# Kernel optimization log

Measured on AMD Instinct MI355X. Metric: run time of the kernel, lower is better.

The kernel has to match this reference:

```python
import jax, jax.numpy as jnp
import numpy as np

N_NODES = 50000
N_EDGES = 400000
NODE_FEAT = 32
HIDDEN = 256
ACTION_DIM = 6
NUM_GRAPHS = 64


def setup_inputs() -> dict:
    key = jax.random.key(0)
    ks = jax.random.split(key, 9)
    x = jax.random.normal(ks[0], (N_NODES, NODE_FEAT), dtype=jnp.float32)
    edge_index = jax.random.randint(ks[1], (2, N_EDGES), 0, N_NODES, dtype=jnp.int32)
    batch = jnp.sort(jax.random.randint(ks[2], (N_NODES,), 0, NUM_GRAPHS, dtype=jnp.int32))
    # GCNConv weights (PyG stores Linear without bias + separate bias term;
    # here W is [in, out] so h = x @ W)
    s1 = 1.0 / np.sqrt(NODE_FEAT)
    s2 = 1.0 / np.sqrt(HIDDEN)
    W1 = jax.random.uniform(ks[3], (NODE_FEAT, HIDDEN), jnp.float32, -s1, s1)
    b1 = jnp.zeros((HIDDEN,), jnp.float32)
    W2 = jax.random.uniform(ks[4], (HIDDEN, HIDDEN), jnp.float32, -s2, s2)
    b2 = jnp.zeros((HIDDEN,), jnp.float32)
    Wf = jax.random.uniform(ks[5], (HIDDEN, 2 * ACTION_DIM), jnp.float32, -s2, s2)
    bf = jax.random.uniform(ks[6], (2 * ACTION_DIM,), jnp.float32, -s2, s2)
    return {"x": x, "edge_index": edge_index, "batch": batch,
            "W1": W1, "b1": b1, "W2": W2, "b2": b2, "Wf": Wf, "bf": bf}


def gcn_conv(x, src, dst, deg_inv_sqrt, W, b, num_nodes):
    # PyG GCNConv: h = x @ W, messages h[src] * norm scattered to dst, + bias.
    h = x @ W  # [N, out]
    norm = deg_inv_sqrt[src] * deg_inv_sqrt[dst]  # [E+N]
    msgs = h[src] * norm[:, None]  # [E+N, out]  (dominant memory traffic)
    out = jax.ops.segment_sum(msgs, dst, num_segments=num_nodes)
    return out + b


def reference(x, edge_index, batch, W1, b1, W2, b2, Wf, bf):
    num_nodes = x.shape[0]
    loop = jnp.arange(num_nodes, dtype=edge_index.dtype)
    src = jnp.concatenate([edge_index[0], loop])  # self-loops, PyG default
    dst = jnp.concatenate([edge_index[1], loop])
    deg = jax.ops.segment_sum(jnp.ones_like(dst, dtype=x.dtype), dst,
                              num_segments=num_nodes)  # >=1 due to self-loops
    deg_inv_sqrt = jax.lax.rsqrt(deg)

    h = jax.nn.relu(gcn_conv(x, src, dst, deg_inv_sqrt, W1, b1, num_nodes))
    h = jax.nn.relu(gcn_conv(h, src, dst, deg_inv_sqrt, W2, b2, num_nodes))

    # global_mean_pool over graph ids
    sums = jax.ops.segment_sum(h, batch, num_segments=NUM_GRAPHS)
    counts = jax.ops.segment_sum(jnp.ones((num_nodes,), x.dtype), batch,
                                 num_segments=NUM_GRAPHS)
    pooled = sums / jnp.maximum(counts, 1.0)[:, None]  # [G, HIDDEN]

    mls = pooled @ Wf + bf  # [G, 2*ACTION_DIM]
    mean, log_std = jnp.split(mls, 2, axis=-1)
    std = jnp.exp(jnp.clip(log_std, -20.0, 2.0))
    return mean, std
```

## Files before the change

### kernel.cpp

```cpp
#include <hip/hip_runtime.h>
#include <math.h>

#define NN 50000
#define FEAT 32
#define HID 256
#define NGRAPH 64
#define CAP 64

typedef __attribute__((ext_vector_type(8))) short bfrag;
typedef __attribute__((ext_vector_type(4))) float f32x4;

__device__ __forceinline__ float bf2f(unsigned short u) {
    union { unsigned int i; float f; } v; v.i = ((unsigned int)u) << 16; return v.f;
}
__device__ __forceinline__ unsigned short f2bf(float f) {
    union { float f; unsigned int i; } v; v.f = f;
    unsigned int r = v.i + 0x7fffu + ((v.i >> 16) & 1u);
    return (unsigned short)(r >> 16);
}

__global__ void k_zero(float4* __restrict__ p, int n16) {
    int i = blockIdx.x * blockDim.x + threadIdx.x;
    if (i < n16) p[i] = make_float4(0.f, 0.f, 0.f, 0.f);
}

__global__ void k_setup(const int* __restrict__ src, const int* __restrict__ dst,
                        const int* __restrict__ batch,
                        int* __restrict__ counter, int* __restrict__ csr,
                        int* __restrict__ starts, int E, int N) {
    int e = blockIdx.x * blockDim.x + threadIdx.x;
    if (e < E) {
        int d = dst[e];
        int p = atomicAdd(&counter[d], 1);
        if (p < CAP) csr[d * CAP + p] = src[e];
    }
    if (e < N) {
        int b = batch[e];
        int prev = (e == 0) ? -1 : batch[e - 1];
        if (b != prev) {
            for (int g = prev + 1; g <= b; ++g) starts[g] = e;
        }
        if (e == N - 1) {
            for (int g = b + 1; g <= NGRAPH; ++g) starts[g] = N;
        }
    }
}

__global__ void k_disps(const float* __restrict__ x, const int* __restrict__ cnt,
                        float* __restrict__ dis, unsigned short* __restrict__ xp, int N) {
    int id = blockIdx.x * blockDim.x + threadIdx.x;
    if (id >= N * FEAT) return;
    int node = id >> 5;
    float dn = rsqrtf((float)(cnt[node] + 1));
    if ((id & 31) == 0) dis[node] = dn;
    xp[id] = f2bf(x[id] * dn);
}

__device__ __forceinline__ void pack_w(const float* __restrict__ W,
                                       unsigned short* __restrict__ Wp, int K, int o) {
    int j    = o & 7;
    int lane = (o >> 3) & 63;
    int rest = o >> 9;
    int nst  = K >> 5;
    int ks   = rest & (nst - 1);
    int nb   = rest / nst;
    int n = nb * 16 + (lane & 15);
    int k = ks * 32 + (lane >> 4) * 8 + j;
    Wp[o] = f2bf(W[(size_t)k * HID + n]);
}
__global__ void k_cvtw(const float* __restrict__ W1, const float* __restrict__ W2,
                       unsigned short* __restrict__ W1p, unsigned short* __restrict__ W2p) {
    int o = blockIdx.x * blockDim.x + threadIdx.x;
    if (o < FEAT * HID) pack_w(W1, W1p, FEAT, o);
    int o2 = o - FEAT * HID;
    if (o2 >= 0 && o2 < HID * HID) pack_w(W2, W2p, HID, o2);
}

__global__ void k_aggx(const unsigned short* __restrict__ xp, const int* __restrict__ cnt,
                       const int* __restrict__ csr, const float* __restrict__ dis,
                       unsigned short* __restrict__ out, int N) {
    int node = blockIdx.x * 8 + (threadIdx.x >> 5);
    if (node >= N) return;
    int col = threadIdx.x & 31;
    float acc = bf2f(xp[(size_t)node * FEAT + col]);
    int e = cnt[node]; if (e > CAP) e = CAP;
    const int* lst = &csr[(size_t)node * CAP];
    int i = 0;
    for (; i + 4 <= e; i += 4) {
        int4 s4 = *(const int4*)&lst[i];
        float v0 = bf2f(xp[(size_t)s4.x * FEAT + col]);
        float v1 = bf2f(xp[(size_t)s4.y * FEAT + col]);
        float v2 = bf2f(xp[(size_t)s4.z * FEAT + col]);
        float v3 = bf2f(xp[(size_t)s4.w * FEAT + col]);
        acc += (v0 + v1) + (v2 + v3);
    }
    for (; i < e; ++i) acc += bf2f(xp[(size_t)lst[i] * FEAT + col]);
    out[(size_t)node * FEAT + col] = f2bf(acc * dis[node]);
}

__global__ void k_aggh(const unsigned short* __restrict__ h, const int* __restrict__ cnt,
                       const int* __restrict__ csr, const float* __restrict__ dis,
                       unsigned short* __restrict__ out, int N) {
    int wid = (int)((blockIdx.x * (size_t)blockDim.x + threadIdx.x) >> 6);
    if (wid >= N) return;
    int lane = threadIdx.x & 63;
    int c0 = lane * 4;

    ushort4 hv = *(const ushort4*)&h[(size_t)wid * HID + c0];
    float a0 = bf2f(hv.x), a1 = bf2f(hv.y), a2 = bf2f(hv.z), a3 = bf2f(hv.w);

    int e = cnt[wid]; if (e > CAP) e = CAP;
    const int* lst = &csr[(size_t)wid * CAP];
    int i = 0;
    for (; i + 8 <= e; i += 8) {
        int4 sa = *(const int4*)&lst[i];
        int4 sb = *(const int4*)&lst[i + 4];
        ushort4 v0 = *(const ushort4*)&h[(size_t)sa.x * HID + c0];
        ushort4 v1 = *(const ushort4*)&h[(size_t)sa.y * HID + c0];
        ushort4 v2 = *(const ushort4*)&h[(size_t)sa.z * HID + c0];
        ushort4 v3 = *(const ushort4*)&h[(size_t)sa.w * HID + c0];
        ushort4 v4 = *(const ushort4*)&h[(size_t)sb.x * HID + c0];
        ushort4 v5 = *(const ushort4*)&h[(size_t)sb.y * HID + c0];
        ushort4 v6 = *(const ushort4*)&h[(size_t)sb.z * HID + c0];
        ushort4 v7 = *(const ushort4*)&h[(size_t)sb.w * HID + c0];
        a0 += ((bf2f(v0.x) + bf2f(v1.x)) + (bf2f(v2.x) + bf2f(v3.x)))
            + ((bf2f(v4.x) + bf2f(v5.x)) + (bf2f(v6.x) + bf2f(v7.x)));
        a1 += ((bf2f(v0.y) + bf2f(v1.y)) + (bf2f(v2.y) + bf2f(v3.y)))
            + ((bf2f(v4.y) + bf2f(v5.y)) + (bf2f(v6.y) + bf2f(v7.y)));
        a2 += ((bf2f(v0.z) + bf2f(v1.z)) + (bf2f(v2.z) + bf2f(v3.z)))
            + ((bf2f(v4.z) + bf2f(v5.z)) + (bf2f(v6.z) + bf2f(v7.z)));
        a3 += ((bf2f(v0.w) + bf2f(v1.w)) + (bf2f(v2.w) + bf2f(v3.w)))
            + ((bf2f(v4.w) + bf2f(v5.w)) + (bf2f(v6.w) + bf2f(v7.w)));
    }
    for (; i + 4 <= e; i += 4) {
        int4 s4 = *(const int4*)&lst[i];
        ushort4 v0 = *(const ushort4*)&h[(size_t)s4.x * HID + c0];
        ushort4 v1 = *(const ushort4*)&h[(size_t)s4.y * HID + c0];
        ushort4 v2 = *(const ushort4*)&h[(size_t)s4.z * HID + c0];
        ushort4 v3 = *(const ushort4*)&h[(size_t)s4.w * HID + c0];
        a0 += (bf2f(v0.x) + bf2f(v1.x)) + (bf2f(v2.x) + bf2f(v3.x));
        a1 += (bf2f(v0.y) + bf2f(v1.y)) + (bf2f(v2.y) + bf2f(v3.y));
        a2 += (bf2f(v0.z) + bf2f(v1.z)) + (bf2f(v2.z) + bf2f(v3.z));
        a3 += (bf2f(v0.w) + bf2f(v1.w)) + (bf2f(v2.w) + bf2f(v3.w));
    }
    for (; i < e; ++i) {
        ushort4 v = *(const ushort4*)&h[(size_t)lst[i] * HID + c0];
        a0 += bf2f(v.x); a1 += bf2f(v.y); a2 += bf2f(v.z); a3 += bf2f(v.w);
    }
    float dn = dis[wid];
    ushort4 o;
    o.x = f2bf(a0 * dn); o.y = f2bf(a1 * dn); o.z = f2bf(a2 * dn); o.w = f2bf(a3 * dn);
    *(ushort4*)&out[(size_t)wid * HID + c0] = o;
}

__global__ __launch_bounds__(256, 4)
void k_mmf(const unsigned short* __restrict__ A, const unsigned short* __restrict__ Wp,
           const float* __restrict__ bias, const float* __restrict__ scale,
           unsigned short* __restrict__ C, int M, int K, int lgK) {
    __shared__ unsigned short lds[64 * 264];
    int tid  = threadIdx.x;
    int lane = tid & 63;
    int wid  = tid >> 6;
    int l15  = lane & 15;
    int lq   = lane >> 4;
    int row0 = blockIdx.x * 64;

    const int P = K + 8;
    int iters = (64 * K) >> 11;
    for (int it = 0; it < iters; ++it) {
        int flat = (it * 256 + tid) * 8;
        int row = flat >> lgK;
        int col = flat & (K - 1);
        bfrag v = {0, 0, 0, 0, 0, 0, 0, 0};
        int gr = row0 + row;
        if (gr < M) v = *(const bfrag*)&A[(size_t)gr * K + col];
        *(bfrag*)&lds[row * P + col] = v;
    }
    __syncthreads();

    int nsteps = K >> 5;
    f32x4 acc[4][4];
#pragma unroll
    for (int mi = 0; mi < 4; ++mi)
#pragma unroll
        for (int ni = 0; ni < 4; ++ni) acc[mi][ni] = (f32x4){0.f, 0.f, 0.f, 0.f};

    for (int ks = 0; ks < nsteps; ++ks) {
        bfrag fb[4];
#pragma unroll
        for (int ni = 0; ni < 4; ++ni) {
            size_t off = (((size_t)(wid * 4 + ni) * nsteps + ks) * 64 + lane) * 8;
            fb[ni] = *(const bfrag*)&Wp[off];
        }
        bfrag fa[4];
        int koff = ks * 32 + lq * 8;
#pragma unroll
        for (int mi = 0; mi < 4; ++mi)
            fa[mi] = *(const bfrag*)&lds[(mi * 16 + l15) * P + koff];
#pragma unroll
        for (int mi = 0; mi < 4; ++mi)
#pragma unroll
            for (int ni = 0; ni < 4; ++ni)
                acc[mi][ni] = __builtin_amdgcn_mfma_f32_16x16x32_bf16(fb[ni], fa[mi], acc[mi][ni], 0, 0, 0);
    }

    float4 bv[4];
#pragma unroll
    for (int ni = 0; ni < 4; ++ni)
        bv[ni] = *(const float4*)&bias[(wid * 4 + ni) * 16 + lq * 4];
    float sv[4];
#pragma unroll
    for (int mi = 0; mi < 4; ++mi) {
        int gr = row0 + mi * 16 + l15;
        sv[mi] = (gr < M) ? scale[gr] : 0.f;
    }

    __syncthreads();
#pragma unroll
    for (int mi = 0; mi < 4; ++mi) {
#pragma unroll
        for (int ni = 0; ni < 4; ++ni) {
            const float* bp = (const float*)&bv[ni];
            ushort4 o;
            o.x = f2bf(fmaxf(acc[mi][ni][0] + bp[0], 0.f) * sv[mi]);
            o.y = f2bf(fmaxf(acc[mi][ni][1] + bp[1], 0.f) * sv[mi]);
            o.z = f2bf(fmaxf(acc[mi][ni][2] + bp[2], 0.f) * sv[mi]);
            o.w = f2bf(fmaxf(acc[mi][ni][3] + bp[3], 0.f) * sv[mi]);
            *(ushort4*)&lds[(mi * 16 + l15) * 264 + (wid * 4 + ni) * 16 + lq * 4] = o;
        }
    }
    __syncthreads();

#pragma unroll
    for (int i = 0; i < 8; ++i) {
        int F = (i * 256 + tid) * 8;
        int row = F >> 8;
        int col = F & 255;
        int gr = row0 + row;
        if (gr < M) {
            bfrag v = *(const bfrag*)&lds[row * 264 + col];
            *(bfrag*)&C[(size_t)gr * HID + col] = v;
        }
    }
}

__global__ __launch_bounds__(256, 4)
void k_mmfp(const unsigned short* __restrict__ A, const unsigned short* __restrict__ Wp,
            const float* __restrict__ bias, const int* __restrict__ batch,
            float* __restrict__ pooled, int M) {
    __shared__ unsigned short lds[64 * 264];
    __shared__ int bshare[64];
    const int K = HID;
    int tid  = threadIdx.x;
    int lane = tid & 63;
    int wid  = tid >> 6;
    int l15  = lane & 15;
    int lq   = lane >> 4;
    int row0 = blockIdx.x * 64;

    if (tid < 64) {
        int gr = row0 + tid;
        bshare[tid] = (gr < M) ? batch[gr] : -1;
    }

    const int P = K + 8;
    for (int it = 0; it < 8; ++it) {
        int flat = (it * 256 + tid) * 8;
        int row = flat >> 8;
        int col = flat & 255;
        bfrag v = {0, 0, 0, 0, 0, 0, 0, 0};
        int gr = row0 + row;
        if (gr < M) v = *(const bfrag*)&A[(size_t)gr * K + col];
        *(bfrag*)&lds[row * P + col] = v;
    }
    __syncthreads();

    f32x4 acc[4][4];
#pragma unroll
    for (int mi = 0; mi < 4; ++mi)
#pragma unroll
        for (int ni = 0; ni < 4; ++ni) acc[mi][ni] = (f32x4){0.f, 0.f, 0.f, 0.f};

    for (int ks = 0; ks < 8; ++ks) {
        bfrag fb[4];
#pragma unroll
        for (int ni = 0; ni < 4; ++ni) {
            size_t off = (((size_t)(wid * 4 + ni) * 8 + ks) * 64 + lane) * 8;
            fb[ni] = *(const bfrag*)&Wp[off];
        }
        bfrag fa[4];
        int koff = ks * 32 + lq * 8;
#pragma unroll
        for (int mi = 0; mi < 4; ++mi)
            fa[mi] = *(const bfrag*)&lds[(mi * 16 + l15) * P + koff];
#pragma unroll
        for (int mi = 0; mi < 4; ++mi)
#pragma unroll
            for (int ni = 0; ni < 4; ++ni)
                acc[mi][ni] = __builtin_amdgcn_mfma_f32_16x16x32_bf16(fb[ni], fa[mi], acc[mi][ni], 0, 0, 0);
    }

    float4 bv[4];
#pragma unroll
    for (int ni = 0; ni < 4; ++ni)
        bv[ni] = *(const float4*)&bias[(wid * 4 + ni) * 16 + lq * 4];

    __syncthreads();
#pragma unroll
    for (int mi = 0; mi < 4; ++mi) {
#pragma unroll
        for (int ni = 0; ni < 4; ++ni) {
            const float* bp = (const float*)&bv[ni];
            ushort4 o;
            o.x = f2bf(fmaxf(acc[mi][ni][0] + bp[0], 0.f));
            o.y = f2bf(fmaxf(acc[mi][ni][1] + bp[1], 0.f));
            o.z = f2bf(fmaxf(acc[mi][ni][2] + bp[2], 0.f));
            o.w = f2bf(fmaxf(acc[mi][ni][3] + bp[3], 0.f));
            *(ushort4*)&lds[(mi * 16 + l15) * 264 + (wid * 4 + ni) * 16 + lq * 4] = o;
        }
    }
    __syncthreads();

    int c = tid;
    float pacc = 0.f;
    int cur = bshare[0];
    for (int r = 0; r < 64; ++r) {
        int g = bshare[r];
        if (g != cur) {
            if (cur >= 0) atomicAdd(&pooled[(size_t)cur * HID + c], pacc);
            pacc = 0.f; cur = g;
        }
        pacc += bf2f(lds[r * 264 + c]);
    }
    if (cur >= 0) atomicAdd(&pooled[(size_t)cur * HID + c], pacc);
}

__global__ void k_head(const float* __restrict__ pooled, const int* __restrict__ starts,
                       const float* __restrict__ Wf, const float* __restrict__ bf,
                       float* __restrict__ out) {
    int t = blockIdx.x * blockDim.x + threadIdx.x;
    if (t >= NGRAPH * 12) return;
    int g = t / 12, j = t % 12;
    float cntf = (float)(starts[g + 1] - starts[g]);
    float inv = 1.f / fmaxf(cntf, 1.f);
    float s = 0.f;
    for (int k = 0; k < HID; ++k) s += pooled[(size_t)g * HID + k] * Wf[k * 12 + j];
    s = s * inv + bf[j];
    if (j < 6) {
        out[g * 6 + j] = s;
    } else {
        float ls = fminf(fmaxf(s, -20.f), 2.f);
        out[NGRAPH * 6 + g * 6 + (j - 6)] = expf(ls);
    }
}

extern "C" void kernel_launch(void* const* d_in, const int* in_sizes, int n_in,
                              void* d_out, int out_size, void* d_ws, size_t ws_size,
                              hipStream_t stream) {
    const float* x     = (const float*)d_in[0];
    const int*   ei    = (const int*)d_in[1];
    const int*   batch = (const int*)d_in[2];
    const float* W1    = (const float*)d_in[3];
    const float* b1    = (const float*)d_in[4];
    const float* W2    = (const float*)d_in[5];
    const float* b2    = (const float*)d_in[6];
    const float* Wf    = (const float*)d_in[7];
    const float* bfv   = (const float*)d_in[8];
    float* out = (float*)d_out;

    const int E = in_sizes[1] / 2;
    const int N = in_sizes[2];
    const int* srcp = ei;
    const int* dstp = ei + E;

    char* ws = (char*)d_ws;
    const size_t OFF_CTR    = 0;
    const size_t OFF_POOLED = 200192;
    const size_t ZERO_BYTES = 265728;
    const size_t OFF_STARTS = 265728;
    const size_t OFF_DIS    = 266240;
    const size_t OFF_W1P    = 466432;
    const size_t OFF_W2P    = 482816;
    const size_t OFF_CSR    = 613888;
    const size_t OFF_XP     = 13413888;
    const size_t OFF_AGGX   = 16613888;
    const size_t OFF_H1     = 19813888;
    const size_t OFF_G      = 45413888;

    int*            ctr    = (int*)(ws + OFF_CTR);
    float*          pooled = (float*)(ws + OFF_POOLED);
    int*            starts = (int*)(ws + OFF_STARTS);
    float*          dis    = (float*)(ws + OFF_DIS);
    unsigned short* W1p    = (unsigned short*)(ws + OFF_W1P);
    unsigned short* W2p    = (unsigned short*)(ws + OFF_W2P);
    int*            csr    = (int*)(ws + OFF_CSR);
    unsigned short* xp     = (unsigned short*)(ws + OFF_XP);
    unsigned short* aggX   = (unsigned short*)(ws + OFF_AGGX);
    unsigned short* h1     = (unsigned short*)(ws + OFF_H1);
    unsigned short* g      = (unsigned short*)(ws + OFF_G);

    const int T = 256;
    k_zero<<<(265728 / 16 + T - 1) / T, T, 0, stream>>>((float4*)ws, 265728 / 16);
    k_setup<<<(E + T - 1) / T, T, 0, stream>>>(srcp, dstp, batch, ctr, csr, starts, E, N);
    k_disps<<<(N * FEAT + T - 1) / T, T, 0, stream>>>(x, ctr, dis, xp, N);
    k_cvtw<<<((FEAT + HID) * HID + T - 1) / T, T, 0, stream>>>(W1, W2, W1p, W2p);

    k_aggx<<<(N + 7) / 8, T, 0, stream>>>(xp, ctr, csr, dis, aggX, N);
    k_mmf<<<(N + 63) / 64, T, 0, stream>>>(aggX, W1p, b1, dis, h1, N, FEAT, 5);

    k_aggh<<<(N * 64 + T - 1) / T, T, 0, stream>>>(h1, ctr, csr, dis, g, N);
    k_mmfp<<<(N + 63) / 64, T, 0, stream>>>(g, W2p, b2, batch, pooled, N);

    k_head<<<3, T, 0, stream>>>(pooled, starts, Wf, bfv, out);
}
```

Baseline: 128.4 us.

## Fuse neighbor aggregation into GEMM kernels and merge zero with weight packing

Moves the gather-sum aggregation for both GCN layers directly into the MFMA GEMM kernels, writing the aggregated rows straight into LDS instead of round-tripping them through global buffers. It also folds the workspace zeroing into the weight-packing kernel, which cuts the launch count. Memory traffic for the intermediate aggX and g buffers and two launches go away. The trade-off is that the fused kernels run with only 782 blocks, and the gather latency now sits ahead of the MFMA work inside each block, so latency hiding and parallelism for the memory-bound gather may get worse.

Result: slower. 138.8 us (+8.1%).

```diff
diff --git a/kernel.cpp b/kernel.cpp
--- a/kernel.cpp
+++ b/kernel.cpp
@@ -17,43 +17,6 @@
     union { float f; unsigned int i; } v; v.f = f;
     unsigned int r = v.i + 0x7fffu + ((v.i >> 16) & 1u);
     return (unsigned short)(r >> 16);
-}
-
-__global__ void k_zero(float4* __restrict__ p, int n16) {
-    int i = blockIdx.x * blockDim.x + threadIdx.x;
-    if (i < n16) p[i] = make_float4(0.f, 0.f, 0.f, 0.f);
-}
-
-__global__ void k_setup(const int* __restrict__ src, const int* __restrict__ dst,
-                        const int* __restrict__ batch,
-                        int* __restrict__ counter, int* __restrict__ csr,
-                        int* __restrict__ starts, int E, int N) {
-    int e = blockIdx.x * blockDim.x + threadIdx.x;
-    if (e < E) {
-        int d = dst[e];
-        int p = atomicAdd(&counter[d], 1);
-        if (p < CAP) csr[d * CAP + p] = src[e];
-    }
-    if (e < N) {
-        int b = batch[e];
-        int prev = (e == 0) ? -1 : batch[e - 1];
-        if (b != prev) {
-            for (int g = prev + 1; g <= b; ++g) starts[g] = e;
-        }
-        if (e == N - 1) {
-            for (int g = b + 1; g <= NGRAPH; ++g) starts[g] = N;
-        }
-    }
-}
-
-__global__ void k_disps(const float* __restrict__ x, const int* __restrict__ cnt,
-                        float* __restrict__ dis, unsigned short* __restrict__ xp, int N) {
-    int id = blockIdx.x * blockDim.x + threadIdx.x;
-    if (id >= N * FEAT) return;
-    int node = id >> 5;
-    float dn = rsqrtf((float)(cnt[node] + 1));
-    if ((id & 31) == 0) dis[node] = dn;
-    xp[id] = f2bf(x[id] * dn);
 }
 
 __device__ __forceinline__ void pack_w(const float* __restrict__ W,
@@ -68,95 +31,54 @@
     int k = ks * 32 + (lane >> 4) * 8 + j;
     Wp[o] = f2bf(W[(size_t)k * HID + n]);
 }
-__global__ void k_cvtw(const float* __restrict__ W1, const float* __restrict__ W2,
+
+__global__ void k_prep(float4* __restrict__ zp, int n16,
+                       const float* __restrict__ W1, const float* __restrict__ W2,
                        unsigned short* __restrict__ W1p, unsigned short* __restrict__ W2p) {
-    int o = blockIdx.x * blockDim.x + threadIdx.x;
-    if (o < FEAT * HID) pack_w(W1, W1p, FEAT, o);
-    int o2 = o - FEAT * HID;
+    int i = blockIdx.x * blockDim.x + threadIdx.x;
+    if (i < n16) zp[i] = make_float4(0.f, 0.f, 0.f, 0.f);
+    if (i < FEAT * HID) pack_w(W1, W1p, FEAT, i);
+    int o2 = i - FEAT * HID;
     if (o2 >= 0 && o2 < HID * HID) pack_w(W2, W2p, HID, o2);
 }
 
-__global__ void k_aggx(const unsigned short* __restrict__ xp, const int* __restrict__ cnt,
-                       const int* __restrict__ csr, const float* __restrict__ dis,
-                       unsigned short* __restrict__ out, int N) {
-    int node = blockIdx.x * 8 + (threadIdx.x >> 5);
-    if (node >= N) return;
-    int col = threadIdx.x & 31;
-    float acc = bf2f(xp[(size_t)node * FEAT + col]);
-    int e = cnt[node]; if (e > CAP) e = CAP;
-    const int* lst = &csr[(size_t)node * CAP];
-    int i = 0;
-    for (; i + 4 <= e; i += 4) {
-        int4 s4 = *(const int4*)&lst[i];
-        float v0 = bf2f(xp[(size_t)s4.x * FEAT + col]);
-        float v1 = bf2f(xp[(size_t)s4.y * FEAT + col]);
-        float v2 = bf2f(xp[(size_t)s4.z * FEAT + col]);
-        float v3 = bf2f(xp[(size_t)s4.w * FEAT + col]);
-        acc += (v0 + v1) + (v2 + v3);
-    }
-    for (; i < e; ++i) acc += bf2f(xp[(size_t)lst[i] * FEAT + col]);
-    out[(size_t)node * FEAT + col] = f2bf(acc * dis[node]);
-}
-
-__global__ void k_aggh(const unsigned short* __restrict__ h, const int* __restrict__ cnt,
-                       const int* __restrict__ csr, const float* __restrict__ dis,
-                       unsigned short* __restrict__ out, int N) {
-    int wid = (int)((blockIdx.x * (size_t)blockDim.x + threadIdx.x) >> 6);
-    if (wid >= N) return;
-    int lane = threadIdx.x & 63;
-    int c0 = lane * 4;
-
-    ushort4 hv = *(const ushort4*)&h[(size_t)wid * HID + c0];
-    float a0 = bf2f(hv.x), a1 = bf2f(hv.y), a2 = bf2f(hv.z), a3 = bf2f(hv.w);
-
-    int e = cnt[wid]; if (e > CAP) e = CAP;
-    const int* lst = &csr[(size_t)wid * CAP];
-    int i = 0;
-    for (; i + 8 <= e; i += 8) {
-        int4 sa = *(const int4*)&lst[i];
-        int4 sb = *(const int4*)&lst[i + 4];
-        ushort4 v0 = *(const ushort4*)&h[(size_t)sa.x * HID + c0];
-        ushort4 v1 = *(const ushort4*)&h[(size_t)sa.y * HID + c0];
-        ushort4 v2 = *(const ushort4*)&h[(size_t)sa.z * HID + c0];
-        ushort4 v3 = *(const ushort4*)&h[(size_t)sa.w * HID + c0];
-        ushort4 v4 = *(const ushort4*)&h[(size_t)sb.x * HID + c0];
-        ushort4 v5 = *(const ushort4*)&h[(size_t)sb.y * HID + c0];
-        ushort4 v6 = *(const ushort4*)&h[(size_t)sb.z * HID + c0];
-        ushort4 v7 = *(const ushort4*)&h[(size_t)sb.w * HID + c0];
-        a0 += ((bf2f(v0.x) + bf2f(v1.x)) + (bf2f(v2.x) + bf2f(v3.x)))
-            + ((bf2f(v4.x) + bf2f(v5.x)) + (bf2f(v6.x) + bf2f(v7.x)));
-        a1 += ((bf2f(v0.y) + bf2f(v1.y)) + (bf2f(v2.y) + bf2f(v3.y)))
-            + ((bf2f(v4.y) + bf2f(v5.y)) + (bf2f(v6.y) + bf2f(v7.y)));
-        a2 += ((bf2f(v0.z) + bf2f(v1.z)) + (bf2f(v2.z) + bf2f(v3.z)))
-            + ((bf2f(v4.z) + bf2f(v5.z)) + (bf2f(v6.z) + bf2f(v7.z)));
-        a3 += ((bf2f(v0.w) + bf2f(v1.w)) + (bf2f(v2.w) + bf2f(v3.w)))
-            + ((bf2f(v4.w) + bf2f(v5.w)) + (bf2f(v6.w) + bf2f(v7.w)));
-    }
-    for (; i + 4 <= e; i += 4) {
-        int4 s4 = *(const int4*)&lst[i];
-        ushort4 v0 = *(const ushort4*)&h[(size_t)s4.x * HID + c0];
-        ushort4 v1 = *(const ushort4*)&h[(size_t)s4.y * HID + c0];
-        ushort4 v2 = *(const ushort4*)&h[(size_t)s4.z * HID + c0];
-        ushort4 v3 = *(const ushort4*)&h[(size_t)s4.w * HID + c0];
-        a0 += (bf2f(v0.x) + bf2f(v1.x)) + (bf2f(v2.x) + bf2f(v3.x));
-        a1 += (bf2f(v0.y) + bf2f(v1.y)) + (bf2f(v2.y) + bf2f(v3.y));
-        a2 += (bf2f(v0.z) + bf2f(v1.z)) + (bf2f(v2.z) + bf2f(v3.z));
-        a3 += (bf2f(v0.w) + bf2f(v1.w)) + (bf2f(v2.w) + bf2f(v3.w));
-    }
-    for (; i < e; ++i) {
-        ushort4 v = *(const ushort4*)&h[(size_t)lst[i] * HID + c0];
-        a0 += bf2f(v.x); a1 += bf2f(v.y); a2 += bf2f(v.z); a3 += bf2f(v.w);
-    }
-    float dn = dis[wid];
-    ushort4 o;
-    o.x = f2bf(a0 * dn); o.y = f2bf(a1 * dn); o.z = f2bf(a2 * dn); o.w = f2bf(a3 * dn);
-    *(ushort4*)&out[(size_t)wid * HID + c0] = o;
+__global__ void k_setup(const int* __restrict__ src, const int* __restrict__ dst,
+                        const int* __restrict__ batch,
+                        int* __restrict__ counter, int* __restrict__ csr,
+                        int* __restrict__ starts, int E, int N) {
+    int e = blockIdx.x * blockDim.x + threadIdx.x;
+    if (e < E) {
+        int d = dst[e];
+        int p = atomicAdd(&counter[d], 1);
+        if (p < CAP) csr[d * CAP + p] = src[e];
+    }
+    if (e < N) {
+        int b = batch[e];
+        int prev = (e == 0) ? -1 : batch[e - 1];
+        if (b != prev) {
+            for (int g = prev + 1; g <= b; ++g) starts[g] = e;
+        }
+        if (e == N - 1) {
+            for (int g = b + 1; g <= NGRAPH; ++g) starts[g] = N;
+        }
+    }
+}
+
+__global__ void k_disps(const float* __restrict__ x, const int* __restrict__ cnt,
+                        float* __restrict__ dis, unsigned short* __restrict__ xp, int N) {
+    int id = blockIdx.x * blockDim.x + threadIdx.x;
+    if (id >= N * FEAT) return;
+    int node = id >> 5;
+    float dn = rsqrtf((float)(cnt[node] + 1));
+    if ((id & 31) == 0) dis[node] = dn;
+    xp[id] = f2bf(x[id] * dn);
 }
 
 __global__ __launch_bounds__(256, 4)
-void k_mmf(const unsigned short* __restrict__ A, const unsigned short* __restrict__ Wp,
-           const float* __restrict__ bias, const float* __restrict__ scale,
-           unsigned short* __restrict__ C, int M, int K, int lgK) {
+void k_fmm1(const unsigned short* __restrict__ xp, const int* __restrict__ cnt,
+            const int* __restrict__ csr, const float* __restrict__ dis,
+            const unsigned short* __restrict__ Wp, const float* __restrict__ bias,
+            unsigned short* __restrict__ C, int M) {
     __shared__ unsigned short lds[64 * 264];
     int tid  = threadIdx.x;
     int lane = tid & 63;
@@ -165,44 +87,51 @@
     int lq   = lane >> 4;
     int row0 = blockIdx.x * 64;
 
-    const int P = K + 8;
-    int iters = (64 * K) >> 11;
-    for (int it = 0; it < iters; ++it) {
-        int flat = (it * 256 + tid) * 8;
-        int row = flat >> lgK;
-        int col = flat & (K - 1);
-        bfrag v = {0, 0, 0, 0, 0, 0, 0, 0};
+    const int PA = 40;
+    int col = tid & 31;
+#pragma unroll
+    for (int rr = 0; rr < 8; ++rr) {
+        int row = rr * 8 + (tid >> 5);
         int gr = row0 + row;
-        if (gr < M) v = *(const bfrag*)&A[(size_t)gr * K + col];
-        *(bfrag*)&lds[row * P + col] = v;
-    }
-    __syncthreads();
-
-    int nsteps = K >> 5;
+        float acc = 0.f;
+        if (gr < M) {
+            acc = bf2f(xp[(size_t)gr * FEAT + col]);
+            int e = cnt[gr]; if (e > CAP) e = CAP;
+            const int* lst = &csr[(size_t)gr * CAP];
+            int i = 0;
+            for (; i + 4 <= e; i += 4) {
+                int4 s4 = *(const int4*)&lst[i];
+                acc += (bf2f(xp[(size_t)s4.x * FEAT + col]) + bf2f(xp[(size_t)s4.y * FEAT + col]))
+                     + (bf2f(xp[(size_t)s4.z * FEAT + col]) + bf2f(xp[(size_t)s4.w * FEAT + col]));
+            }
+            for (; i < e; ++i) acc += bf2f(xp[(size_t)lst[i] * FEAT + col]);
+            acc *= dis[gr];
+        }
+        lds[row * PA + col] = f2bf(acc);
+    }
+    __syncthreads();
+
     f32x4 acc[4][4];
 #pragma unroll
     for (int mi = 0; mi < 4; ++mi)
 #pragma unroll
         for (int ni = 0; ni < 4; ++ni) acc[mi][ni] = (f32x4){0.f, 0.f, 0.f, 0.f};
 
-    for (int ks = 0; ks < nsteps; ++ks) {
-        bfrag fb[4];
-#pragma unroll
-        for (int ni = 0; ni < 4; ++ni) {
-            size_t off = (((size_t)(wid * 4 + ni) * nsteps + ks) * 64 + lane) * 8;
-            fb[ni] = *(const bfrag*)&Wp[off];
-        }
-        bfrag fa[4];
-        int koff = ks * 32 + lq * 8;
-#pragma unroll
-        for (int mi = 0; mi < 4; ++mi)
-            fa[mi] = *(const bfrag*)&lds[(mi * 16 + l15) * P + koff];
-#pragma unroll
-        for (int mi = 0; mi < 4; ++mi)
-#pragma unroll
-            for (int ni = 0; ni < 4; ++ni)
-                acc[mi][ni] = __builtin_amdgcn_mfma_f32_16x16x32_bf16(fb[ni], fa[mi], acc[mi][ni], 0, 0, 0);
-    }
+    bfrag fb[4];
+#pragma unroll
+    for (int ni = 0; ni < 4; ++ni) {
+        size_t off = (((size_t)(wid * 4 + ni)) * 64 + lane) * 8;
+        fb[ni] = *(const bfrag*)&Wp[off];
+    }
+    bfrag fa[4];
+#pragma unroll
+    for (int mi = 0; mi < 4; ++mi)
+        fa[mi] = *(const bfrag*)&lds[(mi * 16 + l15) * PA + lq * 8];
+#pragma unroll
+    for (int mi = 0; mi < 4; ++mi)
+#pragma unroll
+        for (int ni = 0; ni < 4; ++ni)
+            acc[mi][ni] = __builtin_amdgcn_mfma_f32_16x16x32_bf16(fb[ni], fa[mi], acc[mi][ni], 0, 0, 0);
 
     float4 bv[4];
 #pragma unroll
@@ -212,7 +141,7 @@
 #pragma unroll
     for (int mi = 0; mi < 4; ++mi) {
         int gr = row0 + mi * 16 + l15;
-        sv[mi] = (gr < M) ? scale[gr] : 0.f;
+        sv[mi] = (gr < M) ? dis[gr] : 0.f;
     }
 
     __syncthreads();
@@ -235,22 +164,22 @@
     for (int i = 0; i < 8; ++i) {
         int F = (i * 256 + tid) * 8;
         int row = F >> 8;
-        int col = F & 255;
+        int c = F & 255;
         int gr = row0 + row;
         if (gr < M) {
-            bfrag v = *(const bfrag*)&lds[row * 264 + col];
-            *(bfrag*)&C[(size_t)gr * HID + col] = v;
+            bfrag v = *(const bfrag*)&lds[row * 264 + c];
+            *(bfrag*)&C[(size_t)gr * HID + c] = v;
         }
     }
 }
 
 __global__ __launch_bounds__(256, 4)
-void k_mmfp(const unsigned short* __restrict__ A, const unsigned short* __restrict__ Wp,
-            const float* __restrict__ bias, const int* __restrict__ batch,
-            float* __restrict__ pooled, int M) {
+void k_fmm2(const unsigned short* __restrict__ h, const int* __restrict__ cnt,
+            const int* __restrict__ csr, const float* __restrict__ dis,
+            const unsigned short* __restrict__ Wp, const float* __restrict__ bias,
+            const int* __restrict__ batch, float* __restrict__ pooled, int M) {
     __shared__ unsigned short lds[64 * 264];
     __shared__ int bshare[64];
-    const int K = HID;
     int tid  = threadIdx.x;
     int lane = tid & 63;
     int wid  = tid >> 6;
@@ -263,15 +192,59 @@
         bshare[tid] = (gr < M) ? batch[gr] : -1;
     }
 
-    const int P = K + 8;
-    for (int it = 0; it < 8; ++it) {
-        int flat = (it * 256 + tid) * 8;
-        int row = flat >> 8;
-        int col = flat & 255;
-        bfrag v = {0, 0, 0, 0, 0, 0, 0, 0};
+    const int PA = 264;
+    int c0 = lane * 4;
+    for (int rr = 0; rr < 16; ++rr) {
+        int row = wid * 16 + rr;
         int gr = row0 + row;
-        if (gr < M) v = *(const bfrag*)&A[(size_t)gr * K + col];
-        *(bfrag*)&lds[row * P + col] = v;
+        float a0 = 0.f, a1 = 0.f, a2 = 0.f, a3 = 0.f;
+        if (gr < M) {
+            ushort4 hv = *(const ushort4*)&h[(size_t)gr * HID + c0];
+            a0 = bf2f(hv.x); a1 = bf2f(hv.y); a2 = bf2f(hv.z); a3 = bf2f(hv.w);
+            int e = cnt[gr]; if (e > CAP) e = CAP;
+            const int* lst = &csr[(size_t)gr * CAP];
+            int i = 0;
+            for (; i + 8 <= e; i += 8) {
+                int4 sa = *(const int4*)&lst[i];
+                int4 sb = *(const int4*)&lst[i + 4];
+                ushort4 v0 = *(const ushort4*)&h[(size_t)sa.x * HID + c0];
+                ushort4 v1 = *(const ushort4*)&h[(size_t)sa.y * HID + c0];
+                ushort4 v2 = *(const ushort4*)&h[(size_t)sa.z * HID + c0];
+                ushort4 v3 = *(const ushort4*)&h[(size_t)sa.w * HID + c0];
+                ushort4 v4 = *(const ushort4*)&h[(size_t)sb.x * HID + c0];
+                ushort4 v5 = *(const ushort4*)&h[(size_t)sb.y * HID + c0];
+                ushort4 v6 = *(const ushort4*)&h[(size_t)sb.z * HID + c0];
+                ushort4 v7 = *(const ushort4*)&h[(size_t)sb.w * HID + c0];
+                a0 += ((bf2f(v0.x) + bf2f(v1.x)) + (bf2f(v2.x) + bf2f(v3.x)))
+                    + ((bf2f(v4.x) + bf2f(v5.x)) + (bf2f(v6.x) + bf2f(v7.x)));
+                a1 += ((bf2f(v0.y) + bf2f(v1.y)) + (bf2f(v2.y) + bf2f(v3.y)))
+                    + ((bf2f(v4.y) + bf2f(v5.y)) + (bf2f(v6.y) + bf2f(v7.y)));
+                a2 += ((bf2f(v0.z) + bf2f(v1.z)) + (bf2f(v2.z) + bf2f(v3.z)))
+                    + ((bf2f(v4.z) + bf2f(v5.z)) + (bf2f(v6.z) + bf2f(v7.z)));
+                a3 += ((bf2f(v0.w) + bf2f(v1.w)) + (bf2f(v2.w) + bf2f(v3.w)))
+                    + ((bf2f(v4.w) + bf2f(v5.w)) + (bf2f(v6.w) + bf2f(v7.w)));
+            }
+            for (; i + 4 <= e; i += 4) {
+                int4 s4 = *(const int4*)&lst[i];
+                ushort4 v0 = *(const ushort4*)&h[(size_t)s4.x * HID + c0];
+                ushort4 v1 = *(const ushort4*)&h[(size_t)s4.y * HID + c0];
+                ushort4 v2 = *(const ushort4*)&h[(size_t)s4.z * HID + c0];
+                ushort4 v3 = *(const ushort4*)&h[(size_t)s4.w * HID + c0];
+                a0 += (bf2f(v0.x) + bf2f(v1.x)) + (bf2f(v2.x) + bf2f(v3.x));
+                a1 += (bf2f(v0.y) + bf2f(v1.y)) + (bf2f(v2.y) + bf2f(v3.y));
+                a2 += (bf2f(v0.z) + bf2f(v1.z)) + (bf2f(v2.z) + bf2f(v3.z));
+                a3 += (bf2f(v0.w) + bf2f(v1.w)) + (bf2f(v2.w) + bf2f(v3.w));
+            }
+            for (; i < e; ++i) {
+                ushort4 v = *(const ushort4*)&h[(size_t)lst[i] * HID + c0];
+                a0 += bf2f(v.x); a1 += bf2f(v.y); a2 += bf2f(v.z); a3 += bf2f(v.w);
+            }
+            float dn = dis[gr];
+            a0 *= dn; a1 *= dn; a2 *= dn; a3 *= dn;
+        }
+        ushort4 o;
+        o.x = f2bf(a0); o.y = f2bf(a1); o.z = f2bf(a2); o.w = f2bf(a3);
+        *(ushort4*)&lds[row * PA + c0] = o;
     }
     __syncthreads();
 
@@ -292,7 +265,7 @@
         int koff = ks * 32 + lq * 8;
 #pragma unroll
         for (int mi = 0; mi < 4; ++mi)
-            fa[mi] = *(const bfrag*)&lds[(mi * 16 + l15) * P + koff];
+            fa[mi] = *(const bfrag*)&lds[(mi * 16 + l15) * PA + koff];
 #pragma unroll
         for (int mi = 0; mi < 4; ++mi)
 #pragma unroll
@@ -383,9 +356,7 @@
     const size_t OFF_W2P    = 482816;
     const size_t OFF_CSR    = 613888;
     const size_t OFF_XP     = 13413888;
-    const size_t OFF_AGGX   = 16613888;
-    const size_t OFF_H1     = 19813888;
-    const size_t OFF_G      = 45413888;
+    const size_t OFF_H1     = 16613888;
 
     int*            ctr    = (int*)(ws + OFF_CTR);
     float*          pooled = (float*)(ws + OFF_POOLED);
@@ -395,21 +366,17 @@
     unsigned short* W2p    = (unsigned short*)(ws + OFF_W2P);
     int*            csr    = (int*)(ws + OFF_CSR);
     unsigned short* xp     = (unsigned short*)(ws + OFF_XP);
-    unsigned short* aggX   = (unsigned short*)(ws + OFF_AGGX);
     unsigned short* h1     = (unsigned short*)(ws + OFF_H1);
-    unsigned short* g      = (unsigned short*)(ws + OFF_G);
 
     const int T = 256;
-    k_zero<<<(265728 / 16 + T - 1) / T, T, 0, stream>>>((float4*)ws, 265728 / 16);
+    const int prep_n = (FEAT + HID) * HID;
+    k_prep<<<(prep_n + T - 1) / T, T, 0, stream>>>((float4*)ws, 265728 / 16, W1, W2, W1p, W2p);
     k_setup<<<(E + T - 1) / T, T, 0, stream>>>(srcp, dstp, batch, ctr, csr, starts, E, N);
     k_disps<<<(N * FEAT + T - 1) / T, T, 0, stream>>>(x, ctr, dis, xp, N);
-    k_cvtw<<<((FEAT + HID) * HID + T - 1) / T, T, 0, stream>>>(W1, W2, W1p, W2p);
-
-    k_aggx<<<(N + 7) / 8, T, 0, stream>>>(xp, ctr, csr, dis, aggX, N);
-    k_mmf<<<(N + 63) / 64, T, 0, stream>>>(aggX, W1p, b1, dis, h1, N, FEAT, 5);
-
-    k_aggh<<<(N * 64 + T - 1) / T, T, 0, stream>>>(h1, ctr, csr, dis, g, N);
-    k_mmfp<<<(N + 63) / 64, T, 0, stream>>>(g, W2p, b2, batch, pooled, N);
+
+    k_fmm1<<<(N + 63) / 64, T, 0, stream>>>(xp, ctr, csr, dis, W1p, b1, h1, N);
+
+    k_fmm2<<<(N + 63) / 64, T, 0, stream>>>(h1, ctr, csr, dis, W2p, b2, batch, pooled, N);
 
     k_head<<<3, T, 0, stream>>>(pooled, starts, Wf, bfv, out);
 }
```
